# Performance work log

Measured on AMD Instinct MI355X. Metric: run time of the kernel, lower is better.

Reference implementation:

```python
import jax, jax.numpy as jnp
import numpy as np

B, DIM, T, H = 8, 1024, 2048, 16
HD = DIM // H  # per-head channel dim = 64


def _toeplitz(v):
    # v: (H, T) -> (H, T, T) with M[h, i, j] = v[h, j - i] if j >= i else 0
    m = v.shape[-1]
    i = jnp.arange(m)[:, None]
    j = jnp.arange(m)[None, :]
    idx = jnp.where(j >= i, j - i, 0)
    return jnp.where(j >= i, v[..., idx], jnp.zeros((), v.dtype))


def setup_inputs() -> dict:
    key = jax.random.key(0)
    ks = jax.random.split(key, 5)
    s = 1.0 / np.sqrt(DIM)
    return {
        "x": jax.random.normal(ks[0], (B, DIM, T), jnp.float32),
        "w_in": jax.random.normal(ks[1], (DIM, DIM), jnp.float32) * s,
        "b_in": jnp.zeros((DIM,), jnp.float32),
        "w_out": jax.random.normal(ks[2], (DIM, DIM), jnp.float32) * s,
        "b_out": jnp.zeros((DIM,), jnp.float32),
        "toep_w": jax.random.normal(ks[3], (H, T), jnp.float32) * 0.02,
        "toep_b": jnp.zeros((H, T), jnp.float32),
    }


def reference(x, w_in, b_in, w_out, b_out, toep_w, toep_b):
    # x: (B, DIM, T) -> (B, T, DIM)
    xt = jnp.transpose(x, (0, 2, 1))
    h1 = xt @ w_in.T + b_in  # (B, T, DIM)
    # (B, T, H*HD) -> (B, H, HD, T)
    p = jnp.transpose(h1.reshape(B, T, H, HD), (0, 2, 3, 1))
    M = _toeplitz(toep_w)  # (H, T, T)
    # bmm with per-head causal Toeplitz matrix + per-head bias over time
    conv = jnp.einsum("bhdt,htu->bhdu", p, M) + toep_b[None, :, None, :]
    # (B, H, HD, T) -> (B, T, H*HD)
    merged = jnp.transpose(conv, (0, 3, 1, 2)).reshape(B, T, DIM)
    out = merged @ w_out.T + b_out  # (B, T, DIM)
    return jnp.transpose(out, (0, 2, 1))  # (B, DIM, T)
```

## Files before the change

### kernel.cpp

```cpp
#include <hip/hip_runtime.h>
#include <hip/hip_bf16.h>
#include <stdint.h>

#define B_   8
#define DIM  1024
#define T_   2048
#define H_   16
#define HD   64

typedef __attribute__((ext_vector_type(8))) short bf16x8;
typedef __attribute__((ext_vector_type(4))) float f32x4;
typedef __attribute__((ext_vector_type(4))) unsigned short u16x4;

__device__ __forceinline__ unsigned short f2bf(float f) {
    union { float f; unsigned u; } v{f};
    unsigned r = v.u + 0x7fffu + ((v.u >> 16) & 1u);
    return (unsigned short)(r >> 16);
}

__device__ __forceinline__ void gl_lds16(const unsigned short* g, unsigned short* l) {
    __builtin_amdgcn_global_load_lds(
        (const __attribute__((address_space(1))) void*)(const void*)g,
        (__attribute__((address_space(3))) void*)(void*)l,
        16, 0, 0);
}

__device__ __forceinline__ bf16x8 ld_frag(const unsigned short* smem, int row, int cg) {
    return *reinterpret_cast<const bf16x8*>(smem + row * 64 + (((cg) ^ (row & 7)) << 3));
}

__global__ void xpose_cast(const float* __restrict__ x, unsigned short* __restrict__ xt) {
    __shared__ float tile[64][65];
    const int b = blockIdx.z;
    const int d0 = blockIdx.y * 64, t0 = blockIdx.x * 64;
    const int tid = threadIdx.x;
    const int c = tid & 63;
    const int r0 = tid >> 6;

    const float* xp = x + ((size_t)b * DIM + d0) * T_ + t0;
#pragma unroll
    for (int i = 0; i < 16; ++i) {
        int r = r0 + i * 4;
        tile[r][c] = xp[(size_t)r * T_ + c];
    }
    __syncthreads();
    unsigned short* op = xt + ((size_t)b * T_ + t0) * DIM + d0;
    const int ci = (tid & 15) * 4;
    const int rr = tid >> 4;
#pragma unroll
    for (int i = 0; i < 4; ++i) {
        int r = rr + i * 16;
        u16x4 v;
#pragma unroll
        for (int j = 0; j < 4; ++j) v[j] = f2bf(tile[ci + j][r]);
        *reinterpret_cast<u16x4*>(op + (size_t)r * DIM + ci) = v;
    }
}

__global__ void cast_weights(const float* __restrict__ w_in, const float* __restrict__ w_out,
                             const float* __restrict__ tw,
                             unsigned short* __restrict__ w_in_b, unsigned short* __restrict__ w_out_b,
                             unsigned short* __restrict__ tw_b) {
    int i = blockIdx.x * 256 + threadIdx.x;
    if (i < DIM * DIM) {
        w_in_b[i]  = f2bf(w_in[i]);
        w_out_b[i] = f2bf(w_out[i]);
    }
    if (i < H_ * T_) tw_b[i] = f2bf(tw[i]);
}

__global__ void gen_mfrag(const unsigned short* __restrict__ twb, unsigned short* __restrict__ Mf) {
    const int h = blockIdx.y, dg = blockIdx.x;
    const int D = (dg - 1) * 64;
    unsigned short* out = Mf + (((size_t)h * 32 + dg) << 13);
    for (int v = threadIdx.x; v < 1024; v += 256) {
        int cg = v >> 7, row = v & 127;
        bf16x8 w;
#pragma unroll
        for (int j = 0; j < 8; ++j) {
            int lag = D + row - (cg * 8 + j);
            w[j] = (lag >= 0) ? (short)twb[h * T_ + lag] : (short)0;
        }
        *reinterpret_cast<bf16x8*>(out + (size_t)v * 8) = w;
    }
}

template <bool OUT_BF16>
__global__ void gemm_k(const unsigned short* __restrict__ Aw,
                       const unsigned short* __restrict__ Bm,
                       const float* __restrict__ bias,
                       void* __restrict__ Out) {
    __shared__ __align__(16) unsigned short As[2][128 * 64];
    __shared__ __align__(16) unsigned short Bs[2][128 * 64];

    const int flat = blockIdx.x;
    const int wid  = (flat & 7) * 128 + (flat >> 3);
    const int nx   = wid & 15;
    const int my   = (wid >> 4) & 7;
    const int b    = wid >> 7;

    const int tid = threadIdx.x, lane = tid & 63, wv = tid >> 6;
    const int m0 = my * 128;
    const int n0 = nx * 128;
    const unsigned short* Bb = Bm + (size_t)b * T_ * DIM;

    const int wr = wv >> 1, wc = wv & 1;
    const int lrow = lane & 15, lg = lane >> 4;
    const int rsub = lane >> 3;
    const int g = (lane & 7) ^ rsub;

    f32x4 acc[4][4] = {};

    auto STAGE = [&](int kt, int p) {
        const int k0 = kt * 64;
#pragma unroll
        for (int it = 0; it < 4; ++it) {
            int ch = wv * 4 + it;
            int r  = ch * 8 + rsub;
            gl_lds16(Aw + (size_t)(m0 + r) * DIM + k0 + g * 8, &As[p][0] + ch * 512);
            gl_lds16(Bb + (size_t)(n0 + r) * DIM + k0 + g * 8, &Bs[p][0] + ch * 512);
        }
    };

    STAGE(0, 0);
    __syncthreads();

    const int NT = DIM / 64;
    for (int i = 0; i < NT; ++i) {
        const int cur = i & 1;
        if (i + 1 < NT) STAGE(i + 1, cur ^ 1);

        const unsigned short* Ab = &As[cur][0];
        const unsigned short* Bf = &Bs[cur][0];
#pragma unroll
        for (int kk = 0; kk < 2; ++kk) {
            bf16x8 af[4], bfr[4];
#pragma unroll
            for (int mt = 0; mt < 4; ++mt) af[mt]  = ld_frag(Ab, wr * 64 + mt * 16 + lrow, kk * 4 + lg);
#pragma unroll
            for (int nt = 0; nt < 4; ++nt) bfr[nt] = ld_frag(Bf, wc * 64 + nt * 16 + lrow, kk * 4 + lg);
#pragma unroll
            for (int mt = 0; mt < 4; ++mt)
#pragma unroll
                for (int nt = 0; nt < 4; ++nt)
                    acc[mt][nt] = __builtin_amdgcn_mfma_f32_16x16x32_bf16(af[mt], bfr[nt], acc[mt][nt], 0, 0, 0);
        }
        __syncthreads();
    }

    const size_t ob = (size_t)b * DIM * T_;
#pragma unroll
    for (int mt = 0; mt < 4; ++mt) {
        int d = m0 + wr * 64 + mt * 16 + lg * 4;
#pragma unroll
        for (int nt = 0; nt < 4; ++nt) {
            int t = n0 + wc * 64 + nt * 16 + lrow;
#pragma unroll
            for (int r = 0; r < 4; ++r) {
                float v = acc[mt][nt][r] + bias[d + r];
                if constexpr (OUT_BF16)
                    ((unsigned short*)Out)[ob + (size_t)(d + r) * T_ + t] = f2bf(v);
                else
                    ((float*)Out)[ob + (size_t)(d + r) * T_ + t] = v;
            }
        }
    }
}

__global__ void conv4_k(const unsigned short* __restrict__ H1,
                        const unsigned short* __restrict__ Mf,
                        const float* __restrict__ tb,
                        unsigned short* __restrict__ Cb) {
    __shared__ __align__(16) unsigned short Ps[2][64 * 64];

    const int flat = blockIdx.x;
    const int wid  = (flat & 7) * 128 + (flat >> 3);
    const int bx   = wid & 7;
    const int b    = (wid >> 3) & 7;
    const int h    = wid >> 6;

    const int tid = threadIdx.x, lane = tid & 63, wv = tid >> 6;
    const unsigned short* Hb = H1 + ((size_t)b * DIM + h * HD) * T_;
    const unsigned short* Ah = Mf + ((size_t)h * 32) * 8192;

    const int lrow = lane & 15, lg = lane >> 4;
    const int rsub = lane >> 3;
    const int g = (lane & 7) ^ rsub;

    const int aoff = (lg * 128 + wv * 32 + lrow) * 8;

#pragma unroll
    for (int ph = 0; ph < 2; ++ph) {
        const int ut = ph ? bx : (T_ / 128 - 1 - bx);
        const int u0 = ut * 128;
        const int nk = 2 * ut + 2;
        f32x4 acc[2][4] = {};

#pragma unroll
        for (int it = 0; it < 2; ++it) {
            int ch = wv * 2 + it;
            int r  = ch * 8 + rsub;
            gl_lds16(Hb + (size_t)r * T_ + g * 8, &Ps[0][0] + ch * 512);
        }
        __syncthreads();

        for (int kt = 0; kt < nk; ++kt) {
            const int cur = kt & 1;
            if (kt + 1 < nk) {
                const int t0n = (kt + 1) * 64;
#pragma unroll
                for (int it = 0; it < 2; ++it) {
                    int ch = wv * 2 + it;
                    int r  = ch * 8 + rsub;
                    gl_lds16(Hb + (size_t)r * T_ + t0n + g * 8, &Ps[cur ^ 1][0] + ch * 512);
                }
            }
            const int dg = 2 * ut - kt + 1;
            const unsigned short* At = Ah + (size_t)dg * 8192;
            bf16x8 af0[2], af1[2];
#pragma unroll
            for (int mt = 0; mt < 2; ++mt) {
                af0[mt] = *reinterpret_cast<const bf16x8*>(At + aoff + mt * 128);
                af1[mt] = *reinterpret_cast<const bf16x8*>(At + 4096 + aoff + mt * 128);
            }
            const unsigned short* Pb = &Ps[cur][0];
            bf16x8 bfr[4];
#pragma unroll
            for (int nt = 0; nt < 4; ++nt) bfr[nt] = ld_frag(Pb, nt * 16 + lrow, lg);
#pragma unroll
            for (int mt = 0; mt < 2; ++mt)
#pragma unroll
                for (int nt = 0; nt < 4; ++nt)
                    acc[mt][nt] = __builtin_amdgcn_mfma_f32_16x16x32_bf16(af0[mt], bfr[nt], acc[mt][nt], 0, 0, 0);
#pragma unroll
            for (int nt = 0; nt < 4; ++nt) bfr[nt] = ld_frag(Pb, nt * 16 + lrow, 4 + lg);
#pragma unroll
            for (int mt = 0; mt < 2; ++mt)
#pragma unroll
                for (int nt = 0; nt < 4; ++nt)
                    acc[mt][nt] = __builtin_amdgcn_mfma_f32_16x16x32_bf16(af1[mt], bfr[nt], acc[mt][nt], 0, 0, 0);

            __syncthreads();
        }

        const size_t base = (size_t)b * T_ * DIM + (size_t)h * HD;
#pragma unroll
        for (int mt = 0; mt < 2; ++mt) {
            int u = u0 + wv * 32 + mt * 16 + lg * 4;
            const float* tbp = tb + h * T_ + u;
            float t0v = tbp[0], t1v = tbp[1], t2v = tbp[2], t3v = tbp[3];
#pragma unroll
            for (int nt = 0; nt < 4; ++nt) {
                int d = nt * 16 + lrow;
                size_t p = base + (size_t)u * DIM + d;
                Cb[p]           = f2bf(acc[mt][nt][0] + t0v);
                Cb[p + DIM]     = f2bf(acc[mt][nt][1] + t1v);
                Cb[p + 2 * DIM] = f2bf(acc[mt][nt][2] + t2v);
                Cb[p + 3 * DIM] = f2bf(acc[mt][nt][3] + t3v);
            }
        }
    }
}

extern "C" void kernel_launch(void* const* d_in, const int* in_sizes, int n_in,
                              void* d_out, int out_size, void* d_ws, size_t ws_size,
                              hipStream_t stream) {
    (void)in_sizes; (void)n_in; (void)out_size; (void)ws_size;
    const float* x      = (const float*)d_in[0];
    const float* w_in   = (const float*)d_in[1];
    const float* b_in   = (const float*)d_in[2];
    const float* w_out  = (const float*)d_in[3];
    const float* b_out  = (const float*)d_in[4];
    const float* toep_w = (const float*)d_in[5];
    const float* toep_b = (const float*)d_in[6];

    char* ws = (char*)d_ws;
    unsigned short* XT    = (unsigned short*)(ws);
    unsigned short* H1    = (unsigned short*)(ws + 33554432);
    unsigned short* Cbuf  = (unsigned short*)(ws + 67108864);
    unsigned short* winb  = (unsigned short*)(ws + 100663296);
    unsigned short* woutb = (unsigned short*)(ws + 102760448);
    unsigned short* twb   = (unsigned short*)(ws + 104857600);
    unsigned short* Mfrag = (unsigned short*)(ws + 104923136);

    xpose_cast<<<dim3(T_ / 64, DIM / 64, B_), dim3(256), 0, stream>>>(x, XT);
    cast_weights<<<dim3((DIM * DIM) / 256), dim3(256), 0, stream>>>(w_in, w_out, toep_w, winb, woutb, twb);
    gen_mfrag<<<dim3(32, H_), dim3(256), 0, stream>>>(twb, Mfrag);
    gemm_k<true><<<dim3(1024), dim3(256), 0, stream>>>(winb, XT, b_in, (void*)H1);
    conv4_k<<<dim3(1024), dim3(256), 0, stream>>>(H1, Mfrag, toep_b, Cbuf);
    gemm_k<false><<<dim3(1024), dim3(256), 0, stream>>>(woutb, Cbuf, b_out, d_out);
}
```

Baseline: 155.1 us.

## Pre-pack weights into MFMA fragment layout and load A directly from global

Adds a kernel that reorders the bf16 weight matrices into a per-tile fragment layout, so the GEMM kernels can read A fragments straight from global memory (and L2) as contiguous 16-byte vectors. The A staging into LDS is removed, which halves LDS traffic and shared-memory footprint and may allow higher occupancy. In exchange, A loads now go to global/L2 inside the k-loop with no prefetch, which can expose latency, and two small extra repack launches are added.

```diff
diff --git a/kernel.cpp b/kernel.cpp
--- a/kernel.cpp
+++ b/kernel.cpp
@@ -85,12 +85,22 @@
     }
 }
 
+__global__ void gen_wfrag(const unsigned short* __restrict__ Wb, unsigned short* __restrict__ Wf) {
+    const int kt = blockIdx.x, my = blockIdx.y;
+    unsigned short* out = Wf + (((size_t)my * 16 + kt) << 13);
+    for (int v = threadIdx.x; v < 1024; v += 256) {
+        int cg = v >> 7, row = v & 127;
+        bf16x8 w = *reinterpret_cast<const bf16x8*>(
+            Wb + (size_t)(my * 128 + row) * DIM + kt * 64 + cg * 8);
+        *reinterpret_cast<bf16x8*>(out + (size_t)v * 8) = w;
+    }
+}
+
 template <bool OUT_BF16>
-__global__ void gemm_k(const unsigned short* __restrict__ Aw,
-                       const unsigned short* __restrict__ Bm,
-                       const float* __restrict__ bias,
-                       void* __restrict__ Out) {
-    __shared__ __align__(16) unsigned short As[2][128 * 64];
+__global__ void gemm2_k(const unsigned short* __restrict__ Wf,
+                        const unsigned short* __restrict__ Bm,
+                        const float* __restrict__ bias,
+                        void* __restrict__ Out) {
     __shared__ __align__(16) unsigned short Bs[2][128 * 64];
 
     const int flat = blockIdx.x;
@@ -102,49 +112,61 @@
     const int tid = threadIdx.x, lane = tid & 63, wv = tid >> 6;
     const int m0 = my * 128;
     const int n0 = nx * 128;
-    const unsigned short* Bb = Bm + (size_t)b * T_ * DIM;
+    const unsigned short* Bb = Bm + (size_t)b * T_ * DIM + (size_t)n0 * DIM;
+    const unsigned short* Aw = Wf + (((size_t)my * 16) << 13);
 
     const int wr = wv >> 1, wc = wv & 1;
     const int lrow = lane & 15, lg = lane >> 4;
     const int rsub = lane >> 3;
     const int g = (lane & 7) ^ rsub;
 
+    const int aoff = (lg * 128 + wr * 64 + lrow) * 8;
+
     f32x4 acc[4][4] = {};
 
-    auto STAGE = [&](int kt, int p) {
+    auto BSTAGE = [&](int kt, int p) {
         const int k0 = kt * 64;
 #pragma unroll
         for (int it = 0; it < 4; ++it) {
             int ch = wv * 4 + it;
             int r  = ch * 8 + rsub;
-            gl_lds16(Aw + (size_t)(m0 + r) * DIM + k0 + g * 8, &As[p][0] + ch * 512);
-            gl_lds16(Bb + (size_t)(n0 + r) * DIM + k0 + g * 8, &Bs[p][0] + ch * 512);
+            gl_lds16(Bb + (size_t)r * DIM + k0 + g * 8, &Bs[p][0] + ch * 512);
         }
     };
 
-    STAGE(0, 0);
+    BSTAGE(0, 0);
     __syncthreads();
 
     const int NT = DIM / 64;
-    for (int i = 0; i < NT; ++i) {
-        const int cur = i & 1;
-        if (i + 1 < NT) STAGE(i + 1, cur ^ 1);
-
-        const unsigned short* Ab = &As[cur][0];
-        const unsigned short* Bf = &Bs[cur][0];
-#pragma unroll
-        for (int kk = 0; kk < 2; ++kk) {
-            bf16x8 af[4], bfr[4];
-#pragma unroll
-            for (int mt = 0; mt < 4; ++mt) af[mt]  = ld_frag(Ab, wr * 64 + mt * 16 + lrow, kk * 4 + lg);
-#pragma unroll
-            for (int nt = 0; nt < 4; ++nt) bfr[nt] = ld_frag(Bf, wc * 64 + nt * 16 + lrow, kk * 4 + lg);
-#pragma unroll
-            for (int mt = 0; mt < 4; ++mt)
-#pragma unroll
-                for (int nt = 0; nt < 4; ++nt)
-                    acc[mt][nt] = __builtin_amdgcn_mfma_f32_16x16x32_bf16(af[mt], bfr[nt], acc[mt][nt], 0, 0, 0);
-        }
+    for (int kt = 0; kt < NT; ++kt) {
+        const int cur = kt & 1;
+        if (kt + 1 < NT) BSTAGE(kt + 1, cur ^ 1);
+
+        const unsigned short* At = Aw + ((size_t)kt << 13);
+        bf16x8 af0[4], af1[4];
+#pragma unroll
+        for (int mt = 0; mt < 4; ++mt) {
+            af0[mt] = *reinterpret_cast<const bf16x8*>(At + aoff + mt * 128);
+            af1[mt] = *reinterpret_cast<const bf16x8*>(At + 4096 + aoff + mt * 128);
+        }
+
+        const unsigned short* Pb = &Bs[cur][0];
+        bf16x8 bfr[4];
+#pragma unroll
+        for (int nt = 0; nt < 4; ++nt) bfr[nt] = ld_frag(Pb, wc * 64 + nt * 16 + lrow, lg);
+#pragma unroll
+        for (int mt = 0; mt < 4; ++mt)
+#pragma unroll
+            for (int nt = 0; nt < 4; ++nt)
+                acc[mt][nt] = __builtin_amdgcn_mfma_f32_16x16x32_bf16(af0[mt], bfr[nt], acc[mt][nt], 0, 0, 0);
+#pragma unroll
+        for (int nt = 0; nt < 4; ++nt) bfr[nt] = ld_frag(Pb, wc * 64 + nt * 16 + lrow, 4 + lg);
+#pragma unroll
+        for (int mt = 0; mt < 4; ++mt)
+#pragma unroll
+            for (int nt = 0; nt < 4; ++nt)
+                acc[mt][nt] = __builtin_amdgcn_mfma_f32_16x16x32_bf16(af1[mt], bfr[nt], acc[mt][nt], 0, 0, 0);
+
         __syncthreads();
     }
 
@@ -282,11 +304,15 @@
     unsigned short* woutb = (unsigned short*)(ws + 102760448);
     unsigned short* twb   = (unsigned short*)(ws + 104857600);
     unsigned short* Mfrag = (unsigned short*)(ws + 104923136);
+    unsigned short* WfI   = (unsigned short*)(ws + 113311744);
+    unsigned short* WfO   = (unsigned short*)(ws + 115408896);
 
     xpose_cast<<<dim3(T_ / 64, DIM / 64, B_), dim3(256), 0, stream>>>(x, XT);
     cast_weights<<<dim3((DIM * DIM) / 256), dim3(256), 0, stream>>>(w_in, w_out, toep_w, winb, woutb, twb);
     gen_mfrag<<<dim3(32, H_), dim3(256), 0, stream>>>(twb, Mfrag);
-    gemm_k<true><<<dim3(1024), dim3(256), 0, stream>>>(winb, XT, b_in, (void*)H1);
+    gen_wfrag<<<dim3(16, 8), dim3(256), 0, stream>>>(winb, WfI);
+    gen_wfrag<<<dim3(16, 8), dim3(256), 0, stream>>>(woutb, WfO);
+    gemm2_k<true><<<dim3(1024), dim3(256), 0, stream>>>(WfI, XT, b_in, (void*)H1);
     conv4_k<<<dim3(1024), dim3(256), 0, stream>>>(H1, Mfrag, toep_b, Cbuf);
-    gemm_k<false><<<dim3(1024), dim3(256), 0, stream>>>(woutb, Cbuf, b_out, d_out);
-}
+    gemm2_k<false><<<dim3(1024), dim3(256), 0, stream>>>(WfO, Cbuf, b_out, d_out);
+}
```

After: 151.5 us. 1.02x faster.
